# Performance work log

Measured on AMD Instinct MI355X. Metric: run time of the kernel, lower is better.

The kernel has to match this reference:

```python
import jax, jax.numpy as jnp
import numpy as np

B, Q, C, H, W, E, HID_ATT, HID_MLP, NUM_CLASSES, NUM_LABELS = 8, 64, 512, 16, 16, 512, 128, 512, 14, 64


def setup_inputs() -> dict:
    key = jax.random.key(0)
    ks = jax.random.split(key, 16)
    s = 0.02
    return {
        "feature": jax.random.normal(ks[0], (B, C, H, W), jnp.float32),
        "label_ids": jax.random.randint(ks[1], (B, Q), 0, NUM_LABELS),
        "query_table": jax.random.normal(ks[2], (NUM_LABELS, E), jnp.float32) * s,
        "W_film": jax.random.normal(ks[3], (E, 2 * C), jnp.float32) * s,
        "b_film": jnp.zeros((2 * C,), jnp.float32),
        "W_att_h": jax.random.normal(ks[4], (C, HID_ATT), jnp.float32) * s,
        "b_att_h": jnp.zeros((HID_ATT,), jnp.float32),
        "W_att_f": jax.random.normal(ks[5], (HID_ATT, 1), jnp.float32) * s,
        "b_att_f": jnp.zeros((1,), jnp.float32),
        "W_mlp1": jax.random.normal(ks[6], (C, HID_MLP), jnp.float32) * s,
        "b_mlp1": jnp.zeros((HID_MLP,), jnp.float32),
        "W_mlp2": jax.random.normal(ks[7], (HID_MLP, NUM_CLASSES), jnp.float32) * s,
        "b_mlp2": jnp.zeros((NUM_CLASSES,), jnp.float32),
    }


def gelu(x):
    return jax.nn.gelu(x, approximate=False)  # torch default GELU is exact erf


def reference(feature, label_ids, query_table, W_film, b_film, W_att_h, b_att_h,
              W_att_f, b_att_f, W_mlp1, b_mlp1, W_mlp2, b_mlp2):
    # query embedding lookup: (B, Q, E)
    qe = query_table[label_ids]
    # flatten spatial: (B, HW, C)
    f = feature.reshape(feature.shape[0], feature.shape[1], -1).transpose(0, 2, 1)
    # FiLM params from queries: (B, Q, 2C) -> gamma, beta (B, Q, C)
    gb = jnp.einsum("bqe,ec->bqc", qe, W_film) + b_film
    gamma, beta = jnp.split(gb, 2, axis=-1)
    # FiLM-modulated features: (B, Q, HW, C)
    film = f[:, None, :, :] * gamma[:, :, None, :] + beta[:, :, None, :]
    # local attention MLP -> sigmoid gate (B, Q, HW, 1)
    hidden = gelu(jnp.einsum("bqnc,ch->bqnh", film, W_att_h) + b_att_h)
    attn = jax.nn.sigmoid(jnp.einsum("bqnh,ho->bqno", hidden, W_att_f) + b_att_f)
    # weighted sum pool over HW, normalized by attention mass
    pooled = (attn * film).sum(axis=2) / (attn.sum(axis=2) + 1e-8)  # (B, Q, C)
    # classification MLP
    logits = jnp.einsum("bqh,ho->bqo", gelu(jnp.einsum("bqc,ch->bqh", pooled, W_mlp1) + b_mlp1), W_mlp2) + b_mlp2
    return logits  # (B, Q, NUM_CLASSES)
```

## Files before the change

kernel.cpp:

```cpp
#include <hip/hip_runtime.h>
#include <hip/hip_bf16.h>

#define B_    8
#define Q_    64
#define C_    512
#define HW_   256
#define E_    512
#define HATT_ 128
#define HMLP_ 512
#define NCLS_ 14
#define NLAB_ 64

typedef unsigned short u16;
typedef unsigned int   u32;
typedef __attribute__((ext_vector_type(8))) short short8;
typedef __attribute__((ext_vector_type(4))) float f32x4;


__device__ __forceinline__ float gelu_fast(float x) {
    const float ax = fabsf(x);
    const float t  = __builtin_amdgcn_rcpf(1.0f + 0.3275911f * ax);
    const float p  = t * (0.254829592f +
                     t * (-0.284496736f +
                     t * (1.421413741f +
                     t * (-1.453152027f +
                     t * 1.061405429f))));
    const float e  = __expf(-x * x);
    const float er = copysignf(1.0f - p * e, x);
    return 0.5f * x * (1.0f + er);
}
__device__ __forceinline__ float sigmoid_(float x) {
    return 1.0f / (1.0f + __expf(-x));
}
__device__ __forceinline__ u16 f2bf(float x) {
    u32 u = __float_as_uint(x);
    u32 r = (u + 0x7fffu + ((u >> 16) & 1u)) >> 16;
    return (u16)r;
}
__device__ __forceinline__ float bf2f(u16 u) {
    return __uint_as_float(((u32)u) << 16);
}
__device__ __forceinline__ void gl2lds16(const void* gsrc, void* ldsdst) {
    __builtin_amdgcn_global_load_lds(
        (const __attribute__((address_space(1))) u32*)gsrc,
        (__attribute__((address_space(3))) u32*)ldsdst, 16, 0, 0);
}

__global__ __launch_bounds__(256) void prep_gbp(
    const float* __restrict__ qt, const float* __restrict__ W_film,
    float* __restrict__ GBp) {
    __shared__ float qrow[128];
    const int bid = blockIdx.x, t = threadIdx.x;
    const int l = bid >> 2, cq = bid & 3;
    if (t < 128) qrow[t] = qt[l * E_ + cq * 128 + t];
    __syncthreads();
    const float* wp = W_film + (size_t)(cq * 128) * 1024 + t * 4;
    f32x4 a = {0.f, 0.f, 0.f, 0.f};
    #pragma unroll 8
    for (int c = 0; c < 128; ++c) {
        const float4 w = *(const float4*)(wp + (size_t)c * 1024);
        const float q = qrow[c];
        a.x += q * w.x; a.y += q * w.y; a.z += q * w.z; a.w += q * w.w;
    }
    *(f32x4*)&GBp[(size_t)bid * 1024 + t * 4] = a;
}

__global__ __launch_bounds__(256) void prep_rest(
    const float* __restrict__ feature, const float* __restrict__ W_mlp1,
    const int* __restrict__ label_ids, const float* __restrict__ b_film,
    const float* __restrict__ W_att_h, const float* __restrict__ GBp,
    u16* __restrict__ W1bf, u16* __restrict__ fT, int* __restrict__ perm,
    float* __restrict__ Gl, float* __restrict__ Bl,
    u16* __restrict__ WgT, float* __restrict__ Dlp) {

    __shared__ __align__(16) char sm[16896];
    const int bid = blockIdx.x, t = threadIdx.x;

    if (bid < 256) {
        float (*tile)[65] = (float(*)[65])sm;
        const int b = bid >> 5, c0 = ((bid >> 2) & 7) * 64, n0 = (bid & 3) * 64;
        const float* fb = feature + (size_t)b * C_ * HW_;
        const int cl = t >> 2, nq = t & 3;
        #pragma unroll
        for (int i = 0; i < 4; ++i) {
            float4 v = *(const float4*)&fb[(c0 + cl) * HW_ + n0 + nq * 16 + i * 4];
            tile[cl][nq * 16 + i * 4 + 0] = v.x;
            tile[cl][nq * 16 + i * 4 + 1] = v.y;
            tile[cl][nq * 16 + i * 4 + 2] = v.z;
            tile[cl][nq * 16 + i * 4 + 3] = v.w;
        }
        __syncthreads();
        const int nl = t >> 2, cqq = t & 3;
        u16 pk[16];
        #pragma unroll
        for (int k = 0; k < 16; ++k) pk[k] = f2bf(tile[cqq * 16 + k][nl]);
        u16* dst = fT + (size_t)(b * HW_ + n0 + nl) * C_ + c0 + cqq * 16;
        *(uint4*)dst       = *(uint4*)pk;
        *(uint4*)(dst + 8) = *(uint4*)(pk + 8);
    } else if (bid < 320) {
        const int b2 = bid - 256;
        #pragma unroll
        for (int k = 0; k < 2; ++k) {
            const int idx = (b2 * 512 + k * 256 + t) * 8;
            float4 v0 = *(const float4*)&W_mlp1[idx];
            float4 v1 = *(const float4*)&W_mlp1[idx + 4];
            u16 pk[8] = {f2bf(v0.x), f2bf(v0.y), f2bf(v0.z), f2bf(v0.w),
                         f2bf(v1.x), f2bf(v1.y), f2bf(v1.z), f2bf(v1.w)};
            *(uint4*)&W1bf[idx] = *(uint4*)pk;
        }
    } else if (bid == 320) {
        int* cnt = (int*)sm;
        if (t < 64) cnt[t] = 0;
        __syncthreads();
        const int l0 = label_ids[t], l1 = label_ids[t + 256];
        atomicAdd(&cnt[l0], 1);
        atomicAdd(&cnt[l1], 1);
        __syncthreads();
        if (t == 0) {
            int run = 0;
            for (int i = 0; i < 64; ++i) { const int c = cnt[i]; cnt[i] = run; run += c; }
        }
        __syncthreads();
        const int p0 = atomicAdd(&cnt[l0], 1);
        perm[p0] = t | (l0 << 16);
        const int p1 = atomicAdd(&cnt[l1], 1);
        perm[p1] = (t + 256) | (l1 << 16);
    } else {
        float* g_s  = (float*)sm;
        float* b_s  = g_s + 128;
        float* dred = b_s + 128;
        const int wb = bid - 321;
        const int l = wb >> 2, cq = wb & 3;

        if (t < 128) {
            const int c = cq * 128 + t;
            float g = b_film[c], be = b_film[512 + c];
            #pragma unroll
            for (int j = 0; j < 4; ++j) {
                g  += GBp[(size_t)(l * 4 + j) * 1024 + c];
                be += GBp[(size_t)(l * 4 + j) * 1024 + 512 + c];
            }
            g_s[t] = g; b_s[t] = be;
            Gl[l * C_ + c] = g;
            Bl[l * C_ + c] = be;
        }
        __syncthreads();

        const int h = t & 127, ch = t >> 7;
        const int hswz = (h >> 1) & 3;
        float dl = 0.f;
        #pragma unroll
        for (int sl = 0; sl < 2; ++sl) {
            const int ss = cq * 4 + ch * 2 + sl;
            char* dst = (char*)WgT + (size_t)l * 131072 + ss * 8192 + h * 64;
            #pragma unroll
            for (int g = 0; g < 4; ++g) {
                u16 pk[8];
                #pragma unroll
                for (int j = 0; j < 8; ++j) {
                    const int cl = ch * 64 + sl * 32 + g * 8 + j;
                    const float w = W_att_h[(size_t)(cq * 128 + cl) * HATT_ + h];
                    pk[j] = f2bf(g_s[cl] * w);
                    dl += b_s[cl] * w;
                }
                *(uint4*)(dst + ((g ^ hswz) * 16)) = *(uint4*)pk;
            }
        }
        dred[t] = dl;
        __syncthreads();
        if (t < 128)
            Dlp[(size_t)(l * 4 + cq) * 128 + t] = dred[t] + dred[128 + t];
    }
}

__global__ __launch_bounds__(256, 4) void attn_gemm(
    const float* __restrict__ W_att_f, const float* __restrict__ b_att_f,
    const float* __restrict__ b_att_h, const float* __restrict__ Dlp,
    const int*   __restrict__ perm,    const u16* __restrict__ WgT,
    const u16*   __restrict__ fT,
    u16* __restrict__ pPb, float* __restrict__ pA) {

    __shared__ __align__(16) char Ash[2][8192];
    __shared__ __align__(16) char Bsh[2][8192];
    __shared__ float d_s[HATT_];
    __shared__ float wf_s[HATT_];
    __shared__ float attn_part[2][128];
    __shared__ float attn_s[128];

    const int t = threadIdx.x;
    const int idx = blockIdx.x;
    const int srank2 = (idx & 7) * 128 + (idx >> 3);
    const int r = srank2 >> 1, nh = srank2 & 1;
    const int pe = perm[r];
    const int bq = pe & 0xffff, l = pe >> 16;
    const int b = bq >> 6;

    if (t < HATT_) {
        d_s[t] = b_att_h[t]
               + Dlp[(size_t)(l * 4 + 0) * 128 + t]
               + Dlp[(size_t)(l * 4 + 1) * 128 + t]
               + Dlp[(size_t)(l * 4 + 2) * 128 + t]
               + Dlp[(size_t)(l * 4 + 3) * 128 + t];
        wf_s[t] = W_att_f[t];
    }

    const u16* fTb = fT + (size_t)b * HW_ * C_ + (size_t)nh * 128 * C_;
    const u16* Wl  = WgT + (size_t)l * 65536;

    const int an0  = t >> 2;
    const int asl0 = (t & 3) ^ ((an0 >> 1) & 3);

    #define STAGE(s_) {                                                       \
        _Pragma("unroll")                                                     \
        for (int it = 0; it < 2; ++it)                                        \
            gl2lds16(fTb + (size_t)(it * 64 + an0) * C_ + (s_) * 32           \
                         + asl0 * 8,                                          \
                     &Ash[(s_) & 1][(it * 256 + t) * 16]);                    \
        _Pragma("unroll")                                                     \
        for (int it = 0; it < 2; ++it)                                        \
            gl2lds16(Wl + (size_t)(s_) * 4096 + (size_t)(it * 256 + t) * 8,   \
                     &Bsh[(s_) & 1][(it * 256 + t) * 16]);                    \
    }

    const int lane = t & 63, w = t >> 6;
    const int wm = w >> 1, wc = w & 1;
    const int lr = lane & 15, lk = lane >> 4;

    const f32x4 zero = {0.f, 0.f, 0.f, 0.f};
    f32x4 acc[4][4];
    #pragma unroll
    for (int mi = 0; mi < 4; ++mi)
        #pragma unroll
        for (int ni = 0; ni < 4; ++ni) acc[mi][ni] = zero;

    STAGE(0);
    __syncthreads();

    #pragma unroll 2
    for (int s = 0; s < 16; ++s) {
        if (s < 15) STAGE(s + 1);
        const char* Ab = Ash[s & 1];
        const char* Bb = Bsh[s & 1];
        short8 af[4], bf[4];
        #pragma unroll
        for (int mi = 0; mi < 4; ++mi) {
            const int nl = wm * 64 + mi * 16 + lr;
            af[mi] = *(const short8*)(Ab + nl * 64 + ((lk ^ ((nl >> 1) & 3)) * 16));
        }
        #pragma unroll
        for (int ni = 0; ni < 4; ++ni) {
            const int h = wc * 64 + ni * 16 + lr;
            bf[ni] = *(const short8*)(Bb + h * 64 + ((lk ^ ((h >> 1) & 3)) * 16));
        }
        #pragma unroll
        for (int mi = 0; mi < 4; ++mi)
            #pragma unroll
            for (int ni = 0; ni < 4; ++ni)
                acc[mi][ni] = __builtin_amdgcn_mfma_f32_16x16x32_bf16(
                    af[mi], bf[ni], acc[mi][ni], 0, 0, 0);
        __syncthreads();
    }

    #pragma unroll
    for (int mi = 0; mi < 4; ++mi) {
        #pragma unroll
        for (int j = 0; j < 4; ++j) {
            float sum = 0.f;
            #pragma unroll
            for (int ni = 0; ni < 4; ++ni) {
                const int h = wc * 64 + ni * 16 + lr;
                sum += gelu_fast(acc[mi][ni][j] + d_s[h]) * wf_s[h];
            }
            sum += __shfl_xor(sum, 1);
            sum += __shfl_xor(sum, 2);
            sum += __shfl_xor(sum, 4);
            sum += __shfl_xor(sum, 8);
            if (lr == 0) attn_part[wc][wm * 64 + mi * 16 + lk * 4 + j] = sum;
        }
    }
    __syncthreads();
    if (t < 128)
        attn_s[t] = sigmoid_(attn_part[0][t] + attn_part[1][t] + b_att_f[0]);
    __syncthreads();
    if (t < 64) {
        float a = attn_s[t] + attn_s[t + 64];
        #pragma unroll
        for (int m = 1; m < 64; m <<= 1) a += __shfl_xor(a, m);
        if (t == 0) pA[bq * 2 + nh] = a;
    }

    float* pred = (float*)Ash;
    {
        const int ng = t >> 7, cb = (t & 127) * 4;
        const u16* fp = fTb + cb;
        f32x4 p = zero;
        #pragma unroll 8
        for (int n = ng * 64; n < ng * 64 + 64; ++n) {
            const uint2 v = *(const uint2*)(fp + (size_t)n * C_);
            const float a = attn_s[n];
            p.x += a * __uint_as_float(v.x << 16);
            p.y += a * __uint_as_float(v.x & 0xffff0000u);
            p.z += a * __uint_as_float(v.y << 16);
            p.w += a * __uint_as_float(v.y & 0xffff0000u);
        }
        *(f32x4*)&pred[ng * 512 + cb] = p;
    }
    __syncthreads();
    {
        const int c0 = t * 2;
        const float v0 = pred[c0]     + pred[512 + c0];
        const float v1 = pred[c0 + 1] + pred[512 + c0 + 1];
        u16 pk[2] = {f2bf(v0), f2bf(v1)};
        *(u32*)&pPb[(size_t)(bq * 2 + nh) * 512 + c0] = *(u32*)pk;
    }
}

__global__ __launch_bounds__(512) void mlp_head(
    const int*   __restrict__ label_ids,
    const float* __restrict__ Gl, const float* __restrict__ Bl,
    const float* __restrict__ b_mlp1, const float* __restrict__ W_mlp2,
    const float* __restrict__ b_mlp2, const u16* __restrict__ pPb,
    const float* __restrict__ pA,     const u16* __restrict__ W1bf,
    float* __restrict__ out) {

    __shared__ float pooled_s[2][C_];
    __shared__ float zred[2][2][HMLP_];
    __shared__ float z_s[2][HMLP_];
    __shared__ float red_s[32 * NCLS_];

    const int t = threadIdx.x;
    const int bq0 = blockIdx.x * 2;

    {
        const int bqi = t >> 8, cc = (t & 255) * 2;
        const int bq = bq0 + bqi, l = label_ids[bq];
        const float A = pA[bq * 2] + pA[bq * 2 + 1];
        const float inv = 1.0f / (A + 1e-8f);
        #pragma unroll
        for (int i = 0; i < 2; ++i) {
            const int c = cc + i;
            const float p = bf2f(pPb[(size_t)(bq * 2) * 512 + c])
                          + bf2f(pPb[(size_t)(bq * 2 + 1) * 512 + c]);
            pooled_s[bqi][c] = (Gl[l * C_ + c] * p + Bl[l * C_ + c] * A) * inv;
        }
    }
    __syncthreads();

    {
        const int hp = t & 255, cg = t >> 8;
        float z00 = 0.f, z01 = 0.f, z10 = 0.f, z11 = 0.f;
        const u16* wp = W1bf + hp * 2;
        #pragma unroll 8
        for (int c = cg * 256; c < cg * 256 + 256; ++c) {
            const u32 v = *(const u32*)(wp + (size_t)c * HMLP_);
            const float w0 = __uint_as_float(v << 16);
            const float w1 = __uint_as_float(v & 0xffff0000u);
            const float pa = pooled_s[0][c], pb = pooled_s[1][c];
            z00 += pa * w0; z01 += pa * w1;
            z10 += pb * w0; z11 += pb * w1;
        }
        float2 a0 = {z00, z01}, a1 = {z10, z11};
        *(float2*)&zred[cg][0][hp * 2] = a0;
        *(float2*)&zred[cg][1][hp * 2] = a1;
    }
    __syncthreads();
    {
        const int bqi = t >> 8, h2 = (t & 255) * 2;
        #pragma unroll
        for (int i = 0; i < 2; ++i) {
            const int h = h2 + i;
            z_s[bqi][h] = gelu_fast(zred[0][bqi][h] + zred[1][bqi][h] + b_mlp1[h]);
        }
    }
    __syncthreads();

    #pragma unroll
    for (int bqi = 0; bqi < 2; ++bqi) {
        if (t < 448) {
            const int o = t % 14, seg = t / 14;
            float s = 0.f;
            #pragma unroll
            for (int k = 0; k < 16; ++k) {
                const int h = seg * 16 + k;
                s += z_s[bqi][h] * W_mlp2[h * NCLS_ + o];
            }
            red_s[seg * NCLS_ + o] = s;
        }
        __syncthreads();
        if (t < NCLS_) {
            float s = b_mlp2[t];
            #pragma unroll
            for (int seg = 0; seg < 32; ++seg) s += red_s[seg * NCLS_ + t];
            out[(bq0 + bqi) * NCLS_ + t] = s;
        }
        __syncthreads();
    }
}

extern "C" void kernel_launch(void* const* d_in, const int* in_sizes, int n_in,
                              void* d_out, int out_size, void* d_ws, size_t ws_size,
                              hipStream_t stream) {
    const float* feature   = (const float*)d_in[0];
    const int*   label_ids = (const int*)  d_in[1];
    const float* qt        = (const float*)d_in[2];
    const float* W_film    = (const float*)d_in[3];
    const float* b_film    = (const float*)d_in[4];
    const float* W_att_h   = (const float*)d_in[5];
    const float* b_att_h   = (const float*)d_in[6];
    const float* W_att_f   = (const float*)d_in[7];
    const float* b_att_f   = (const float*)d_in[8];
    const float* W_mlp1    = (const float*)d_in[9];
    const float* b_mlp1    = (const float*)d_in[10];
    const float* W_mlp2    = (const float*)d_in[11];
    const float* b_mlp2    = (const float*)d_in[12];
    float* out = (float*)d_out;

    char* wsb   = (char*)d_ws;
    float* GBp  = (float*)wsb;
    u16*   pPb  = (u16*)  wsb;
    float* pA   = (float*)(wsb + 1048576);
    int*   perm = (int*)  (wsb + 1052672);
    float* Dlp  = (float*)(wsb + 1054720);
    float* Gl   = (float*)(wsb + 1185792);
    float* Bl   = (float*)(wsb + 1316864);
    u16*   W1bf = (u16*)  (wsb + 1447936);
    u16*   fTp  = (u16*)  (wsb + 1972224);
    u16*   WgT  = (u16*)  (wsb + 4069376);

    hipLaunchKernelGGL(prep_gbp, dim3(256), dim3(256), 0, stream,
                       qt, W_film, GBp);
    hipLaunchKernelGGL(prep_rest, dim3(577), dim3(256), 0, stream,
                       feature, W_mlp1, label_ids, b_film, W_att_h, GBp,
                       W1bf, fTp, perm, Gl, Bl, WgT, Dlp);
    hipLaunchKernelGGL(attn_gemm, dim3(1024), dim3(256), 0, stream,
                       W_att_f, b_att_f, b_att_h, Dlp, perm, WgT, fTp, pPb, pA);
    hipLaunchKernelGGL(mlp_head, dim3(256), dim3(512), 0, stream,
                       label_ids, Gl, Bl, b_mlp1, W_mlp2, b_mlp2,
                       pPb, pA, W1bf, out);
}
```

Measured before the change: 68.50 us.

## Deduplicate identical (batch, label) queries and deepen attention GEMM prefetch

```diff
diff --git a/kernel.cpp b/kernel.cpp
--- a/kernel.cpp
+++ b/kernel.cpp
@@ -69,7 +69,9 @@
     const float* __restrict__ feature, const float* __restrict__ W_mlp1,
     const int* __restrict__ label_ids, const float* __restrict__ b_film,
     const float* __restrict__ W_att_h, const float* __restrict__ GBp,
-    u16* __restrict__ W1bf, u16* __restrict__ fT, int* __restrict__ perm,
+    u16* __restrict__ W1bf, u16* __restrict__ fT,
+    int* __restrict__ sperm, int* __restrict__ uled,
+    int* __restrict__ ustart, int* __restrict__ nuniq,
     float* __restrict__ Gl, float* __restrict__ Bl,
     u16* __restrict__ WgT, float* __restrict__ Dlp) {
 
@@ -109,22 +111,38 @@
             *(uint4*)&W1bf[idx] = *(uint4*)pk;
         }
     } else if (bid == 320) {
-        int* cnt = (int*)sm;
-        if (t < 64) cnt[t] = 0;
-        __syncthreads();
-        const int l0 = label_ids[t], l1 = label_ids[t + 256];
-        atomicAdd(&cnt[l0], 1);
-        atomicAdd(&cnt[l1], 1);
+        int* cnt  = (int*)sm;
+        int* skey = cnt + 512;
+        int* sbq  = skey + 512;
+        cnt[t] = 0; cnt[t + 256] = 0;
+        __syncthreads();
+        const int bqa = t, bqb = t + 256;
+        const int ka = (bqa >> 6) * 64 + label_ids[bqa];
+        const int kb = (bqb >> 6) * 64 + label_ids[bqb];
+        atomicAdd(&cnt[ka], 1);
+        atomicAdd(&cnt[kb], 1);
         __syncthreads();
         if (t == 0) {
             int run = 0;
-            for (int i = 0; i < 64; ++i) { const int c = cnt[i]; cnt[i] = run; run += c; }
-        }
-        __syncthreads();
-        const int p0 = atomicAdd(&cnt[l0], 1);
-        perm[p0] = t | (l0 << 16);
-        const int p1 = atomicAdd(&cnt[l1], 1);
-        perm[p1] = (t + 256) | (l1 << 16);
+            for (int i = 0; i < 512; ++i) { const int c = cnt[i]; cnt[i] = run; run += c; }
+        }
+        __syncthreads();
+        const int pa = atomicAdd(&cnt[ka], 1); skey[pa] = ka; sbq[pa] = bqa;
+        const int pb = atomicAdd(&cnt[kb], 1); skey[pb] = kb; sbq[pb] = bqb;
+        __syncthreads();
+        sperm[t] = sbq[t]; sperm[t + 256] = sbq[t + 256];
+        if (t == 0) {
+            int u = -1;
+            for (int i = 0; i < 512; ++i) {
+                if (i == 0 || skey[i] != skey[i - 1]) {
+                    ++u;
+                    ustart[u] = i;
+                    uled[u] = sbq[i] | ((skey[i] & 63) << 16);
+                }
+            }
+            nuniq[0] = u + 1;
+            for (int j = u + 1; j <= 512; ++j) ustart[j] = 512;
+        }
     } else {
         float* g_s  = (float*)sm;
         float* b_s  = g_s + 128;
@@ -176,8 +194,8 @@
 __global__ __launch_bounds__(256, 4) void attn_gemm(
     const float* __restrict__ W_att_f, const float* __restrict__ b_att_f,
     const float* __restrict__ b_att_h, const float* __restrict__ Dlp,
-    const int*   __restrict__ perm,    const u16* __restrict__ WgT,
-    const u16*   __restrict__ fT,
+    const int*   __restrict__ uled,    const int* __restrict__ nuniq,
+    const u16*   __restrict__ WgT,     const u16* __restrict__ fT,
     u16* __restrict__ pPb, float* __restrict__ pA) {
 
     __shared__ __align__(16) char Ash[2][8192];
@@ -189,10 +207,10 @@
 
     const int t = threadIdx.x;
     const int idx = blockIdx.x;
-    const int srank2 = (idx & 7) * 128 + (idx >> 3);
-    const int r = srank2 >> 1, nh = srank2 & 1;
-    const int pe = perm[r];
-    const int bq = pe & 0xffff, l = pe >> 16;
+    const int u = idx >> 1, nh = idx & 1;
+    if (u >= nuniq[0]) return;
+    const int ul = uled[u];
+    const int bq = ul & 0xffff, l = ul >> 16;
     const int b = bq >> 6;
 
     if (t < HATT_) {
@@ -234,11 +252,13 @@
         for (int ni = 0; ni < 4; ++ni) acc[mi][ni] = zero;
 
     STAGE(0);
-    __syncthreads();
-
-    #pragma unroll 2
+    STAGE(1);
+    asm volatile("s_waitcnt vmcnt(4)" ::: "memory");
+    __builtin_amdgcn_sched_barrier(0);
+    __builtin_amdgcn_s_barrier();
+
+    #pragma unroll
     for (int s = 0; s < 16; ++s) {
-        if (s < 15) STAGE(s + 1);
         const char* Ab = Ash[s & 1];
         const char* Bb = Bsh[s & 1];
         short8 af[4], bf[4];
@@ -252,13 +272,23 @@
             const int h = wc * 64 + ni * 16 + lr;
             bf[ni] = *(const short8*)(Bb + h * 64 + ((lk ^ ((h >> 1) & 3)) * 16));
         }
+        asm volatile("s_waitcnt lgkmcnt(0)" ::: "memory");
+        __builtin_amdgcn_sched_barrier(0);
+        __builtin_amdgcn_s_barrier();
+        if (s < 14) STAGE(s + 2);
         #pragma unroll
         for (int mi = 0; mi < 4; ++mi)
             #pragma unroll
             for (int ni = 0; ni < 4; ++ni)
                 acc[mi][ni] = __builtin_amdgcn_mfma_f32_16x16x32_bf16(
                     af[mi], bf[ni], acc[mi][ni], 0, 0, 0);
-        __syncthreads();
+        if (s < 15) {
+            __builtin_amdgcn_sched_barrier(0);
+            if (s < 14) asm volatile("s_waitcnt vmcnt(4)" ::: "memory");
+            else        asm volatile("s_waitcnt vmcnt(0)" ::: "memory");
+            __builtin_amdgcn_sched_barrier(0);
+            __builtin_amdgcn_s_barrier();
+        }
     }
 
     #pragma unroll
@@ -286,7 +316,7 @@
         float a = attn_s[t] + attn_s[t + 64];
         #pragma unroll
         for (int m = 1; m < 64; m <<= 1) a += __shfl_xor(a, m);
-        if (t == 0) pA[bq * 2 + nh] = a;
+        if (t == 0) pA[u * 2 + nh] = a;
     }
 
     float* pred = (float*)Ash;
@@ -311,12 +341,13 @@
         const float v0 = pred[c0]     + pred[512 + c0];
         const float v1 = pred[c0 + 1] + pred[512 + c0 + 1];
         u16 pk[2] = {f2bf(v0), f2bf(v1)};
-        *(u32*)&pPb[(size_t)(bq * 2 + nh) * 512 + c0] = *(u32*)pk;
+        *(u32*)&pPb[(size_t)(u * 2 + nh) * 512 + c0] = *(u32*)pk;
     }
 }
 
 __global__ __launch_bounds__(512) void mlp_head(
-    const int*   __restrict__ label_ids,
+    const int*   __restrict__ uled,  const int* __restrict__ ustart,
+    const int*   __restrict__ nuniq, const int* __restrict__ sperm,
     const float* __restrict__ Gl, const float* __restrict__ Bl,
     const float* __restrict__ b_mlp1, const float* __restrict__ W_mlp2,
     const float* __restrict__ b_mlp2, const u16* __restrict__ pPb,
@@ -329,19 +360,27 @@
     __shared__ float red_s[32 * NCLS_];
 
     const int t = threadIdx.x;
-    const int bq0 = blockIdx.x * 2;
+    const int u0 = blockIdx.x * 2;
+    const int nu = nuniq[0];
+    if (u0 >= nu) return;
 
     {
-        const int bqi = t >> 8, cc = (t & 255) * 2;
-        const int bq = bq0 + bqi, l = label_ids[bq];
-        const float A = pA[bq * 2] + pA[bq * 2 + 1];
-        const float inv = 1.0f / (A + 1e-8f);
-        #pragma unroll
-        for (int i = 0; i < 2; ++i) {
-            const int c = cc + i;
-            const float p = bf2f(pPb[(size_t)(bq * 2) * 512 + c])
-                          + bf2f(pPb[(size_t)(bq * 2 + 1) * 512 + c]);
-            pooled_s[bqi][c] = (Gl[l * C_ + c] * p + Bl[l * C_ + c] * A) * inv;
+        const int ui = t >> 8, cc = (t & 255) * 2;
+        const int u = u0 + ui;
+        if (u < nu) {
+            const int l = uled[u] >> 16;
+            const float A = pA[u * 2] + pA[u * 2 + 1];
+            const float inv = 1.0f / (A + 1e-8f);
+            #pragma unroll
+            for (int i = 0; i < 2; ++i) {
+                const int c = cc + i;
+                const float p = bf2f(pPb[(size_t)(u * 2) * 512 + c])
+                              + bf2f(pPb[(size_t)(u * 2 + 1) * 512 + c]);
+                pooled_s[ui][c] = (Gl[l * C_ + c] * p + Bl[l * C_ + c] * A) * inv;
+            }
+        } else {
+            pooled_s[ui][cc] = 0.f;
+            pooled_s[ui][cc + 1] = 0.f;
         }
     }
     __syncthreads();
@@ -365,33 +404,36 @@
     }
     __syncthreads();
     {
-        const int bqi = t >> 8, h2 = (t & 255) * 2;
+        const int ui = t >> 8, h2 = (t & 255) * 2;
         #pragma unroll
         for (int i = 0; i < 2; ++i) {
             const int h = h2 + i;
-            z_s[bqi][h] = gelu_fast(zred[0][bqi][h] + zred[1][bqi][h] + b_mlp1[h]);
+            z_s[ui][h] = gelu_fast(zred[0][ui][h] + zred[1][ui][h] + b_mlp1[h]);
         }
     }
     __syncthreads();
 
     #pragma unroll
-    for (int bqi = 0; bqi < 2; ++bqi) {
+    for (int ui = 0; ui < 2; ++ui) {
+        const int u = u0 + ui;
         if (t < 448) {
             const int o = t % 14, seg = t / 14;
             float s = 0.f;
             #pragma unroll
             for (int k = 0; k < 16; ++k) {
                 const int h = seg * 16 + k;
-                s += z_s[bqi][h] * W_mlp2[h * NCLS_ + o];
+                s += z_s[ui][h] * W_mlp2[h * NCLS_ + o];
             }
             red_s[seg * NCLS_ + o] = s;
         }
         __syncthreads();
-        if (t < NCLS_) {
+        if (u < nu && t < NCLS_) {
             float s = b_mlp2[t];
             #pragma unroll
             for (int seg = 0; seg < 32; ++seg) s += red_s[seg * NCLS_ + t];
-            out[(bq0 + bqi) * NCLS_ + t] = s;
+            const int r0 = ustart[u], r1 = ustart[u + 1];
+            for (int r = r0; r < r1; ++r)
+                out[sperm[r] * NCLS_ + t] = s;
         }
         __syncthreads();
     }
@@ -415,26 +457,30 @@
     const float* b_mlp2    = (const float*)d_in[12];
     float* out = (float*)d_out;
 
-    char* wsb   = (char*)d_ws;
-    float* GBp  = (float*)wsb;
-    u16*   pPb  = (u16*)  wsb;
-    float* pA   = (float*)(wsb + 1048576);
-    int*   perm = (int*)  (wsb + 1052672);
-    float* Dlp  = (float*)(wsb + 1054720);
-    float* Gl   = (float*)(wsb + 1185792);
-    float* Bl   = (float*)(wsb + 1316864);
-    u16*   W1bf = (u16*)  (wsb + 1447936);
-    u16*   fTp  = (u16*)  (wsb + 1972224);
-    u16*   WgT  = (u16*)  (wsb + 4069376);
+    char* wsb    = (char*)d_ws;
+    float* GBp   = (float*)wsb;
+    u16*   pPb   = (u16*)  wsb;
+    float* pA    = (float*)(wsb + 1048576);
+    int*   sperm = (int*)  (wsb + 1052672);
+    int*   uled  = (int*)  (wsb + 1054720);
+    int*   ustart= (int*)  (wsb + 1056768);
+    int*   nuniq = (int*)  (wsb + 1060864);
+    float* Dlp   = (float*)(wsb + 1064960);
+    float* Gl    = (float*)(wsb + 1196032);
+    float* Bl    = (float*)(wsb + 1327104);
+    u16*   W1bf  = (u16*)  (wsb + 1458176);
+    u16*   fTp   = (u16*)  (wsb + 1982464);
+    u16*   WgT   = (u16*)  (wsb + 4079616);
 
     hipLaunchKernelGGL(prep_gbp, dim3(256), dim3(256), 0, stream,
                        qt, W_film, GBp);
     hipLaunchKernelGGL(prep_rest, dim3(577), dim3(256), 0, stream,
                        feature, W_mlp1, label_ids, b_film, W_att_h, GBp,
-                       W1bf, fTp, perm, Gl, Bl, WgT, Dlp);
+                       W1bf, fTp, sperm, uled, ustart, nuniq, Gl, Bl, WgT, Dlp);
     hipLaunchKernelGGL(attn_gemm, dim3(1024), dim3(256), 0, stream,
-                       W_att_f, b_att_f, b_att_h, Dlp, perm, WgT, fTp, pPb, pA);
+                       W_att_f, b_att_f, b_att_h, Dlp, uled, nuniq,
+                       WgT, fTp, pPb, pA);
     hipLaunchKernelGGL(mlp_head, dim3(256), dim3(512), 0, stream,
-                       label_ids, Gl, Bl, b_mlp1, W_mlp2, b_mlp2,
-                       pPb, pA, W1bf, out);
-}
+                       uled, ustart, nuniq, sperm, Gl, Bl,
+                       b_mlp1, W_mlp2, b_mlp2, pPb, pA, W1bf, out);
+}
```

Measured after the change: 102.0 us. 1.49x slower.
